# Optimization experiments

Hardware: AMD Instinct MI355X
Metric: run time of the kernel (lower is better)

The kernel has to match this reference:

```python
import jax, jax.numpy as jnp
import numpy as np

D_MODEL = 384
D_INNER = 768
D_STATE = 16
DT_RANK = 24
D_CONV = 4
N_BLOCKS = 6
EPS = 1e-5


def setup_inputs() -> dict:
    key = jax.random.key(0)
    ks = jax.random.split(key, 16)
    s = 0.05
    x = jax.random.normal(ks[0], (1, 8, 16, 16, D_MODEL), jnp.float32)
    inp = {
        'x': x,
        'norm_w': jnp.ones((N_BLOCKS, D_MODEL), jnp.float32),
        'in_proj_w': s * jax.random.normal(ks[1], (N_BLOCKS, 2 * D_INNER, D_MODEL), jnp.float32),
        'conv_w': s * jax.random.normal(ks[2], (N_BLOCKS, D_INNER, D_CONV), jnp.float32),
        'conv_b': jnp.zeros((N_BLOCKS, D_INNER), jnp.float32),
        'x_proj_w': s * jax.random.normal(ks[3], (N_BLOCKS, DT_RANK + 2 * D_STATE, D_INNER), jnp.float32),
        'dt_proj_w': s * jax.random.normal(ks[4], (N_BLOCKS, D_INNER, DT_RANK), jnp.float32),
        'dt_proj_b': jnp.full((N_BLOCKS, D_INNER), -2.0, jnp.float32),  # softplus(-2) ~ small init dt
        'A_log': jnp.broadcast_to(jnp.log(jnp.arange(1, D_STATE + 1, dtype=jnp.float32)), (N_BLOCKS, D_INNER, D_STATE)).copy(),
        'D_param': jnp.ones((N_BLOCKS, D_INNER), jnp.float32),
        'out_proj_w': s * jax.random.normal(ks[5], (N_BLOCKS, D_MODEL, D_INNER), jnp.float32),
    }
    return inp


def _rmsnorm(x, w):
    var = jnp.mean(x * x, axis=-1, keepdims=True)
    return x * jax.lax.rsqrt(var + EPS) * w


def _causal_conv1d(x, w, b):
    # x: (N, L, C), w: (C, k) depthwise, causal left-pad
    xt = jnp.transpose(x, (0, 2, 1))  # (N, C, L)
    out = jax.lax.conv_general_dilated(
        xt, w[:, None, :], window_strides=(1,), padding=[(w.shape[-1] - 1, 0)],
        dimension_numbers=('NCH', 'OIH', 'NCH'), feature_group_count=w.shape[0])
    return jnp.transpose(out, (0, 2, 1)) + b


def _selective_scan(u, delta, A, Bm, Cm, Dp):
    # u, delta: (N, L, d_in); A: (d_in, d_state); Bm, Cm: (N, L, d_state)
    dA = jnp.exp(delta[..., None] * A)                      # (N, L, d_in, d_state)
    dBu = delta[..., None] * Bm[:, :, None, :] * u[..., None]

    def step(h, inp):
        dA_t, dBu_t, C_t = inp
        h = dA_t * h + dBu_t                                # (N, d_in, d_state)
        y = jnp.einsum('nds,ns->nd', h, C_t)
        return h, y

    h0 = jnp.zeros((u.shape[0], u.shape[2], A.shape[1]), u.dtype)
    _, ys = jax.lax.scan(step, h0, (jnp.transpose(dA, (1, 0, 2, 3)),
                                    jnp.transpose(dBu, (1, 0, 2, 3)),
                                    jnp.transpose(Cm, (1, 0, 2))))
    y = jnp.transpose(ys, (1, 0, 2))                        # (N, L, d_in)
    return y + u * Dp


def _mamba_layer(x, p):
    # pre-norm residual Mamba mixer; x: (N, L, D_MODEL)
    h = _rmsnorm(x, p['norm_w'])
    xz = jnp.einsum('nld,ed->nle', h, p['in_proj_w'])       # (N, L, 2*d_inner)
    xp, z = jnp.split(xz, 2, axis=-1)
    xp = jax.nn.silu(_causal_conv1d(xp, p['conv_w'], p['conv_b']))
    x_dbl = jnp.einsum('nld,ed->nle', xp, p['x_proj_w'])
    dt, Bm, Cm = jnp.split(x_dbl, [DT_RANK, DT_RANK + D_STATE], axis=-1)
    dt = jax.nn.softplus(jnp.einsum('nlr,dr->nld', dt, p['dt_proj_w']) + p['dt_proj_b'])
    A = -jnp.exp(p['A_log'])
    y = _selective_scan(xp, dt, A, Bm, Cm, p['D_param'])
    y = y * jax.nn.silu(z)
    return x + jnp.einsum('nle,de->nld', y, p['out_proj_w'])


def _block(x, params, i):
    p = {k: v[i] for k, v in params.items()}
    return _mamba_layer(x, p)


def reference(x, norm_w, in_proj_w, conv_w, conv_b, x_proj_w, dt_proj_w, dt_proj_b, A_log, D_param, out_proj_w):
    params = dict(norm_w=norm_w, in_proj_w=in_proj_w, conv_w=conv_w, conv_b=conv_b,
                  x_proj_w=x_proj_w, dt_proj_w=dt_proj_w, dt_proj_b=dt_proj_b,
                  A_log=A_log, D_param=D_param, out_proj_w=out_proj_w)
    N, L, H, W, D = x.shape
    # HWL ordering
    h = jnp.transpose(x, (0, 2, 3, 1, 4)).reshape(N, H * W * L, D)
    h = _block(h, params, 0)                                 # hwl
    h = _block(h[:, ::-1], params, 1)[:, ::-1]               # r_hwl
    # LWH ordering
    h = h.reshape(N, H, W, L, D)
    h = jnp.transpose(h, (0, 3, 2, 1, 4)).reshape(N, L * W * H, D)
    h = _block(h, params, 2)                                 # lwh
    h = _block(h[:, ::-1], params, 3)[:, ::-1]               # r_lwh
    # LHW ordering
    h = h.reshape(N, L, W, H, D)
    h = jnp.transpose(h, (0, 1, 3, 2, 4)).reshape(N, L * H * W, D)
    h = _block(h, params, 4)                                 # lhw
    h = _block(h[:, ::-1], params, 5)[:, ::-1]               # r_lhw
    return h.reshape(N, L, H, W, D)
```

## Files before the change

kernel.cpp:

```cpp
#include <hip/hip_runtime.h>
#include <math.h>

#define D_MODEL 384
#define D_INNER 768
#define D_STATE 16
#define DT_RANK 24
#define NTOK    2048
#define XDIM    56
#define CHUNK   32
#define NCHUNK  (NTOK / CHUNK)

typedef __attribute__((ext_vector_type(8))) short bf16x8;
typedef __attribute__((ext_vector_type(4))) float f32x4;

__device__ __forceinline__ int tok_of(int order, int p) {
    int q = (order & 1) ? (NTOK - 1 - p) : p;
    int grp = order >> 1;
    int l, h, w;
    if (grp == 0)      { h = q >> 7;  w = (q >> 3) & 15; l = q & 7;  }
    else if (grp == 1) { l = q >> 8;  w = (q >> 4) & 15; h = q & 15; }
    else               { return q; }
    return l * 256 + h * 16 + w;
}

__device__ __forceinline__ float sigmoidf_(float x) { return 1.f / (1.f + expf(-x)); }
__device__ __forceinline__ float softplusf_(float x) { return (x > 20.f) ? x : log1pf(expf(x)); }

__device__ __forceinline__ void bf16split_(float a, unsigned short& hb, unsigned short& lb) {
    unsigned int ab = __float_as_uint(a);
    hb = (unsigned short)(ab >> 16);
    float hf = __uint_as_float(ab & 0xFFFF0000u);
    lb = (unsigned short)(__float_as_uint(a - hf) >> 16);
}

__global__ __launch_bounds__(128) void rmsnorm_gather_k(
    const float* __restrict__ R, const float* __restrict__ nw,
    float* __restrict__ Xn, int order)
{
    const int p   = blockIdx.x;
    const int tok = tok_of(order, p);
    const float* src = R + tok * D_MODEL;
    const int tid = threadIdx.x;
    float v0 = src[tid], v1 = src[tid + 128], v2 = src[tid + 256];
    float ss = v0 * v0 + v1 * v1 + v2 * v2;
#pragma unroll
    for (int off = 32; off > 0; off >>= 1) ss += __shfl_xor(ss, off);
    __shared__ float tot[2];
    if ((tid & 63) == 0) tot[tid >> 6] = ss;
    __syncthreads();
    const float rs = rsqrtf((tot[0] + tot[1]) * (1.f / D_MODEL) + 1e-5f);
    float* dst = Xn + p * D_MODEL;
    dst[tid]       = v0 * rs * nw[tid];
    dst[tid + 128] = v1 * rs * nw[tid + 128];
    dst[tid + 256] = v2 * rs * nw[tid + 256];
}

__global__ __launch_bounds__(256, 3) void inproj_mfma_k(
    const float* __restrict__ Xn, const float* __restrict__ W,
    float* __restrict__ XP, float* __restrict__ GT)
{
    __shared__ __align__(16) short Ah[4 * 64 * 8];
    __shared__ __align__(16) short Al[4 * 64 * 8];
    __shared__ __align__(16) short Bh[4 * 64 * 8];
    __shared__ __align__(16) short Bl[4 * 64 * 8];

    const int tid = threadIdx.x;
    const int m0 = blockIdx.y * 64;
    const int n0 = blockIdx.x * 64;
    const int w  = tid >> 6;
    const int l  = tid & 63;
    const int lr = l & 15;
    const int kg = l >> 4;
    const int srow = tid >> 2;
    const int skq  = tid & 3;

    f32x4 acc[4];
#pragma unroll
    for (int r = 0; r < 4; ++r) acc[r] = (f32x4){0.f, 0.f, 0.f, 0.f};

    for (int k0 = 0; k0 < D_MODEL; k0 += 32) {
        {
            const float* ap = Xn + (m0 + srow) * D_MODEL + k0 + skq * 8;
            const float4 a0 = *(const float4*)ap;
            const float4 a1 = *(const float4*)(ap + 4);
            const float av[8] = {a0.x, a0.y, a0.z, a0.w, a1.x, a1.y, a1.z, a1.w};
            union { bf16x8 v; unsigned short u[8]; } hu, lu;
#pragma unroll
            for (int j = 0; j < 8; ++j) bf16split_(av[j], hu.u[j], lu.u[j]);
            *(bf16x8*)&Ah[(skq * 64 + srow) * 8] = hu.v;
            *(bf16x8*)&Al[(skq * 64 + srow) * 8] = lu.v;

            const float* wp = W + (n0 + srow) * D_MODEL + k0 + skq * 8;
            const float4 w0 = *(const float4*)wp;
            const float4 w1 = *(const float4*)(wp + 4);
            const float wv[8] = {w0.x, w0.y, w0.z, w0.w, w1.x, w1.y, w1.z, w1.w};
            union { bf16x8 v; unsigned short u[8]; } hw, lw;
#pragma unroll
            for (int j = 0; j < 8; ++j) bf16split_(wv[j], hw.u[j], lw.u[j]);
            *(bf16x8*)&Bh[(skq * 64 + srow) * 8] = hw.v;
            *(bf16x8*)&Bl[(skq * 64 + srow) * 8] = lw.v;
        }
        __syncthreads();

        const bf16x8 bh = *(const bf16x8*)&Bh[(kg * 64 + w * 16 + lr) * 8];
        const bf16x8 bl = *(const bf16x8*)&Bl[(kg * 64 + w * 16 + lr) * 8];
#pragma unroll
        for (int r = 0; r < 4; ++r) {
            const bf16x8 ah = *(const bf16x8*)&Ah[(kg * 64 + r * 16 + lr) * 8];
            const bf16x8 al = *(const bf16x8*)&Al[(kg * 64 + r * 16 + lr) * 8];
            acc[r] = __builtin_amdgcn_mfma_f32_16x16x32_bf16(ah, bh, acc[r], 0, 0, 0);
            acc[r] = __builtin_amdgcn_mfma_f32_16x16x32_bf16(ah, bl, acc[r], 0, 0, 0);
            acc[r] = __builtin_amdgcn_mfma_f32_16x16x32_bf16(al, bh, acc[r], 0, 0, 0);
        }
        __syncthreads();
    }

    const int n = n0 + w * 16 + lr;
    if (n0 < D_INNER) {
#pragma unroll
        for (int r = 0; r < 4; ++r)
#pragma unroll
            for (int i = 0; i < 4; ++i) {
                const int t = m0 + r * 16 + kg * 4 + i;
                XP[t * D_INNER + n] = acc[r][i];
            }
    } else {
        const int n2 = n - D_INNER;
#pragma unroll
        for (int r = 0; r < 4; ++r)
#pragma unroll
            for (int i = 0; i < 4; ++i) {
                const int t = m0 + r * 16 + kg * 4 + i;
                const float c = acc[r][i];
                GT[n2 * NTOK + t] = c * sigmoidf_(c);
            }
    }
}

template<int MODE, bool TRANSA>
__global__ __launch_bounds__(256, 2) void gemm_k(
    const float* __restrict__ A, int lda,
    const float* __restrict__ W,
    float* __restrict__ C,
    int M, int N, int K,
    const float* __restrict__ bias,
    float* __restrict__ C2,
    int kspan)
{
    __shared__ float As[16][68];
    __shared__ float Ws[16][68];
    const int tid = threadIdx.x;
    const int m0 = blockIdx.y * 64;
    const int n0 = blockIdx.x * 64;
    const int tx = tid & 15, ty = tid >> 4;
    const int lrow = tid >> 2;
    const int lk   = (tid & 3) << 2;
    const int kb   = blockIdx.z * kspan;
    const int ke   = (kb + kspan < K) ? (kb + kspan) : K;
    float acc[4][4] = {{0.f}};

    for (int k0 = kb; k0 < ke; k0 += 16) {
        if (TRANSA) {
            const int kk = k0 + (tid & 15);
            const int mq = tid >> 4;
            float4 v = make_float4(0.f, 0.f, 0.f, 0.f);
            if (kk < K) v = *(const float4*)&A[kk * lda + m0 + mq * 4];
            *(float4*)&As[tid & 15][mq * 4] = v;
        } else {
            const int m = m0 + lrow;
            const float* src = A + m * lda + (k0 + lk);
            float4 v = make_float4(0.f, 0.f, 0.f, 0.f);
            if (k0 + lk + 3 < K) v = *(const float4*)src;
            else {
                if (k0 + lk + 0 < K) v.x = src[0];
                if (k0 + lk + 1 < K) v.y = src[1];
                if (k0 + lk + 2 < K) v.z = src[2];
            }
            As[lk + 0][lrow] = v.x; As[lk + 1][lrow] = v.y;
            As[lk + 2][lrow] = v.z; As[lk + 3][lrow] = v.w;
        }
        {
            const int n = n0 + lrow;
            float4 u = make_float4(0.f, 0.f, 0.f, 0.f);
            if (n < N) {
                const float* srcw = W + n * K + (k0 + lk);
                if (k0 + lk + 3 < K) u = *(const float4*)srcw;
                else {
                    if (k0 + lk + 0 < K) u.x = srcw[0];
                    if (k0 + lk + 1 < K) u.y = srcw[1];
                    if (k0 + lk + 2 < K) u.z = srcw[2];
                }
            }
            Ws[lk + 0][lrow] = u.x; Ws[lk + 1][lrow] = u.y;
            Ws[lk + 2][lrow] = u.z; Ws[lk + 3][lrow] = u.w;
        }
        __syncthreads();
#pragma unroll
        for (int k = 0; k < 16; ++k) {
            float4 a4 = *(const float4*)&As[k][ty * 4];
            float4 w4 = *(const float4*)&Ws[k][tx * 4];
            float ar[4] = {a4.x, a4.y, a4.z, a4.w};
            float wr[4] = {w4.x, w4.y, w4.z, w4.w};
#pragma unroll
            for (int i = 0; i < 4; ++i)
#pragma unroll
                for (int j = 0; j < 4; ++j)
                    acc[i][j] = fmaf(ar[i], wr[j], acc[i][j]);
        }
        __syncthreads();
    }

    const int row0 = m0 + ty * 4;
    const int col0 = n0 + tx * 4;
    if (MODE == 0) {
        float* Cz = C + (size_t)blockIdx.z * M * N;
#pragma unroll
        for (int i = 0; i < 4; ++i) {
            float4 v = make_float4(acc[i][0], acc[i][1], acc[i][2], acc[i][3]);
            *(float4*)&Cz[(row0 + i) * N + col0] = v;
        }
    } else if (MODE == 3) {
        float* Cz = C + (size_t)blockIdx.z * N * NTOK;
#pragma unroll
        for (int j = 0; j < 4; ++j) {
            const int col = col0 + j;
            if (col < N) {
                float4 v = make_float4(acc[0][j], acc[1][j], acc[2][j], acc[3][j]);
                *(float4*)&Cz[col * NTOK + row0] = v;
            }
        }
    } else if (MODE == 4) {
#pragma unroll
        for (int j = 0; j < 4; ++j) {
            const int col = col0 + j;
            if (col < N) {
                const float bv = bias[col];
                float4 v = make_float4(softplusf_(acc[0][j] + bv), softplusf_(acc[1][j] + bv),
                                       softplusf_(acc[2][j] + bv), softplusf_(acc[3][j] + bv));
                *(float4*)&C[col * NTOK + row0] = v;
            }
        }
    }
}

__global__ __launch_bounds__(256) void reduce_px_k(
    const float* __restrict__ PX, float* __restrict__ XDT)
{
    const int i4 = blockIdx.x * 256 + threadIdx.x;
    float4 s = ((const float4*)PX)[i4];
#pragma unroll
    for (int z = 1; z < 8; ++z) {
        float4 v = ((const float4*)PX)[z * (XDIM * NTOK / 4) + i4];
        s.x += v.x; s.y += v.y; s.z += v.z; s.w += v.w;
    }
    ((float4*)XDT)[i4] = s;
}

__global__ __launch_bounds__(384) void reduce_scatter_k(
    const float* __restrict__ PO, float* __restrict__ R, int order)
{
    const int m = blockIdx.x;
    const int col = threadIdx.x;
    float s = PO[m * D_MODEL + col];
#pragma unroll
    for (int z = 1; z < 4; ++z)
        s += PO[z * (NTOK * D_MODEL) + m * D_MODEL + col];
    const int tok = tok_of(order, m);
    R[tok * D_MODEL + col] += s;
}

__global__ __launch_bounds__(256) void conv_silu_t_k(
    const float* __restrict__ XP, const float* __restrict__ cw,
    const float* __restrict__ cb, float* __restrict__ XCT)
{
    __shared__ float xs[67][33];
    const int c0 = blockIdx.x * 32;
    const int t0 = blockIdx.y * 64;
    const int tid = threadIdx.x;
    const int col = tid & 31, rr = tid >> 5;
#pragma unroll
    for (int r = rr; r < 67; r += 8) {
        const int t = t0 - 3 + r;
        xs[r][col] = (t >= 0) ? XP[t * D_INNER + c0 + col] : 0.f;
    }
    __syncthreads();
    const int tl = tid & 63;
#pragma unroll
    for (int cl = tid >> 6; cl < 32; cl += 4) {
        const int c = c0 + cl;
        const float4 w4 = *(const float4*)(cw + c * 4);
        float acc = cb[c];
        acc = fmaf(w4.x, xs[tl + 0][cl], acc);
        acc = fmaf(w4.y, xs[tl + 1][cl], acc);
        acc = fmaf(w4.z, xs[tl + 2][cl], acc);
        acc = fmaf(w4.w, xs[tl + 3][cl], acc);
        XCT[c * NTOK + t0 + tl] = acc * sigmoidf_(acc);
    }
}

__global__ __launch_bounds__(256) void scan_phase1_k(
    const float* __restrict__ XCT, const float* __restrict__ DTT,
    const float* __restrict__ XDT, const float* __restrict__ A_log,
    float* __restrict__ Aprod, float* __restrict__ Hpart)
{
    const int tid = threadIdx.x;
    const int s = tid & 15;
    const int d = blockIdx.x * 16 + (tid >> 4);
    const int chunk = blockIdx.y;
    const float Aneg = -expf(A_log[d * D_STATE + s]);
    const float* dtp = DTT + d * NTOK + chunk * CHUNK;
    const float* up  = XCT + d * NTOK + chunk * CHUNK;
    const float* Bp  = XDT + (DT_RANK + s) * NTOK + chunk * CHUNK;
    float h = 0.f, ap = 1.f;
#pragma unroll
    for (int tt = 0; tt < CHUNK; tt += 4) {
        const float4 dt4 = *(const float4*)(dtp + tt);
        const float4 u4  = *(const float4*)(up + tt);
        const float4 B4  = *(const float4*)(Bp + tt);
        float a;
        a = expf(dt4.x * Aneg); h = fmaf(a, h, dt4.x * B4.x * u4.x); ap *= a;
        a = expf(dt4.y * Aneg); h = fmaf(a, h, dt4.y * B4.y * u4.y); ap *= a;
        a = expf(dt4.z * Aneg); h = fmaf(a, h, dt4.z * B4.z * u4.z); ap *= a;
        a = expf(dt4.w * Aneg); h = fmaf(a, h, dt4.w * B4.w * u4.w); ap *= a;
    }
    const int idx = (chunk * D_INNER + d) * D_STATE + s;
    Aprod[idx] = ap;
    Hpart[idx] = h;
}

__global__ __launch_bounds__(256) void scan_phase2_k(
    const float* __restrict__ Aprod, const float* __restrict__ Hpart,
    float* __restrict__ Hinit)
{
    const int tid = blockIdx.x * 256 + threadIdx.x;
    float h = 0.f;
#pragma unroll 8
    for (int c = 0; c < NCHUNK; ++c) {
        const int idx = c * (D_INNER * D_STATE) + tid;
        Hinit[idx] = h;
        h = fmaf(Aprod[idx], h, Hpart[idx]);
    }
}

__global__ __launch_bounds__(256) void scan_phase3_k(
    const float* __restrict__ XCT, const float* __restrict__ DTT,
    const float* __restrict__ XDT, const float* __restrict__ GT,
    const float* __restrict__ A_log, const float* __restrict__ Dp,
    const float* __restrict__ Hinit, float* __restrict__ YGT)
{
    const int tid = threadIdx.x;
    const int s = tid & 15;
    const int d = blockIdx.x * 16 + (tid >> 4);
    const int chunk = blockIdx.y;
    const float Aneg = -expf(A_log[d * D_STATE + s]);
    const float Dv = Dp[d];
    const float* dtp = DTT + d * NTOK + chunk * CHUNK;
    const float* up  = XCT + d * NTOK + chunk * CHUNK;
    const float* Bp  = XDT + (DT_RANK + s) * NTOK + chunk * CHUNK;
    const float* Cp  = XDT + (DT_RANK + D_STATE + s) * NTOK + chunk * CHUNK;
    const float* Gp  = GT  + d * NTOK + chunk * CHUNK;
    float* Yp        = YGT + d * NTOK + chunk * CHUNK;
    float h = Hinit[(chunk * D_INNER + d) * D_STATE + s];
#pragma unroll
    for (int tt = 0; tt < CHUNK; tt += 4) {
        const float4 dt4 = *(const float4*)(dtp + tt);
        const float4 u4  = *(const float4*)(up + tt);
        const float4 B4  = *(const float4*)(Bp + tt);
        const float4 C4  = *(const float4*)(Cp + tt);
        float a, p0, p1, p2, p3;
        a = expf(dt4.x * Aneg); h = fmaf(a, h, dt4.x * B4.x * u4.x); p0 = h * C4.x;
        a = expf(dt4.y * Aneg); h = fmaf(a, h, dt4.y * B4.y * u4.y); p1 = h * C4.y;
        a = expf(dt4.z * Aneg); h = fmaf(a, h, dt4.z * B4.z * u4.z); p2 = h * C4.z;
        a = expf(dt4.w * Aneg); h = fmaf(a, h, dt4.w * B4.w * u4.w); p3 = h * C4.w;
#pragma unroll
        for (int m = 1; m <= 8; m <<= 1) {
            p0 += __shfl_xor(p0, m); p1 += __shfl_xor(p1, m);
            p2 += __shfl_xor(p2, m); p3 += __shfl_xor(p3, m);
        }
        if (s == 0) {
            const float4 g4 = *(const float4*)(Gp + tt);
            float4 y;
            y.x = (p0 + u4.x * Dv) * g4.x;
            y.y = (p1 + u4.y * Dv) * g4.y;
            y.z = (p2 + u4.z * Dv) * g4.z;
            y.w = (p3 + u4.w * Dv) * g4.w;
            *(float4*)(Yp + tt) = y;
        }
    }
}

extern "C" void kernel_launch(void* const* d_in, const int* in_sizes, int n_in,
                              void* d_out, int out_size, void* d_ws, size_t ws_size,
                              hipStream_t stream)
{
    const float* x        = (const float*)d_in[0];
    const float* norm_w   = (const float*)d_in[1];
    const float* in_proj  = (const float*)d_in[2];
    const float* conv_w   = (const float*)d_in[3];
    const float* conv_b   = (const float*)d_in[4];
    const float* x_proj   = (const float*)d_in[5];
    const float* dt_proj  = (const float*)d_in[6];
    const float* dt_b     = (const float*)d_in[7];
    const float* A_log    = (const float*)d_in[8];
    const float* D_param  = (const float*)d_in[9];
    const float* out_proj = (const float*)d_in[10];

    float* ws = (float*)d_ws;
    float* R     = ws;
    float* XP    = R   + 786432;
    float* Xn    = XP  + 1572864;
    float* GT    = Xn  + 786432;
    float* XCT   = GT  + 1572864;
    float* XDT   = XCT + 1572864;
    float* DTT   = XDT + 114688;
    float* YGT   = DTT + 1572864;
    float* Aprod = Xn;
    float* Hpart = YGT;
    float* Hinit = XP;
    float* PX    = XP;
    float* PO    = GT;

    hipMemcpyAsync(R, x, (size_t)786432 * sizeof(float), hipMemcpyDeviceToDevice, stream);

    for (int b = 0; b < 6; ++b) {
        rmsnorm_gather_k<<<NTOK, 128, 0, stream>>>(R, norm_w + b * D_MODEL, Xn, b);

        inproj_mfma_k<<<dim3(24, 32), 256, 0, stream>>>(
            Xn, in_proj + (size_t)b * 2 * D_INNER * D_MODEL, XP, GT);

        conv_silu_t_k<<<dim3(24, 32), 256, 0, stream>>>(
            XP, conv_w + b * D_INNER * 4, conv_b + b * D_INNER, XCT);

        gemm_k<3, true><<<dim3(1, 32, 8), 256, 0, stream>>>(
            XCT, NTOK, x_proj + (size_t)b * XDIM * D_INNER, PX,
            NTOK, XDIM, D_INNER, nullptr, nullptr, 96);

        reduce_px_k<<<112, 256, 0, stream>>>(PX, XDT);

        gemm_k<4, true><<<dim3(12, 32, 1), 256, 0, stream>>>(
            XDT, NTOK, dt_proj + (size_t)b * D_INNER * DT_RANK, DTT,
            NTOK, D_INNER, DT_RANK, dt_b + b * D_INNER, nullptr, DT_RANK);

        scan_phase1_k<<<dim3(48, NCHUNK), 256, 0, stream>>>(
            XCT, DTT, XDT, A_log + (size_t)b * D_INNER * D_STATE, Aprod, Hpart);

        scan_phase2_k<<<48, 256, 0, stream>>>(Aprod, Hpart, Hinit);

        scan_phase3_k<<<dim3(48, NCHUNK), 256, 0, stream>>>(
            XCT, DTT, XDT, GT, A_log + (size_t)b * D_INNER * D_STATE,
            D_param + b * D_INNER, Hinit, YGT);

        gemm_k<0, true><<<dim3(6, 32, 4), 256, 0, stream>>>(
            YGT, NTOK, out_proj + (size_t)b * D_MODEL * D_INNER, PO,
            NTOK, D_MODEL, D_INNER, nullptr, nullptr, 192);

        reduce_scatter_k<<<NTOK, 384, 0, stream>>>(PO, R, b);
    }

    hipMemcpyAsync(d_out, R, (size_t)786432 * sizeof(float), hipMemcpyDeviceToDevice, stream);
}
```

Measured before the change: 937.1 us.

## Pre-split weights to bf16 hi/lo and move out_proj to MFMA

Adds a presplit kernel that converts the in_proj and out_proj weights into bf16 high/low pairs once per call. RMSNorm now writes the split activations directly, so the in_proj MFMA kernel only copies bf16 data into shared memory. The out_proj GEMM moves from the fp32 FMA kernel to a new split-bf16 MFMA kernel with split-K of 2 instead of 4. To support that, the scan writes Y token-major, which turns its float4 stores into strided scalar stores, and the extra weight buffers need more workspace.

```diff
diff --git a/kernel.cpp b/kernel.cpp
--- a/kernel.cpp
+++ b/kernel.cpp
@@ -33,9 +33,25 @@
     lb = (unsigned short)(__float_as_uint(a - hf) >> 16);
 }
 
+__global__ __launch_bounds__(256) void presplit_k(
+    const float* __restrict__ A, unsigned short* __restrict__ H,
+    unsigned short* __restrict__ L, int n4)
+{
+    const int i = blockIdx.x * 256 + threadIdx.x;
+    if (i >= n4) return;
+    const float4 v = ((const float4*)A)[i];
+    ushort4 h, l;
+    bf16split_(v.x, h.x, l.x);
+    bf16split_(v.y, h.y, l.y);
+    bf16split_(v.z, h.z, l.z);
+    bf16split_(v.w, h.w, l.w);
+    ((ushort4*)H)[i] = h;
+    ((ushort4*)L)[i] = l;
+}
+
 __global__ __launch_bounds__(128) void rmsnorm_gather_k(
     const float* __restrict__ R, const float* __restrict__ nw,
-    float* __restrict__ Xn, int order)
+    unsigned short* __restrict__ Xnh, unsigned short* __restrict__ Xnl, int order)
 {
     const int p   = blockIdx.x;
     const int tok = tok_of(order, p);
@@ -49,14 +65,18 @@
     if ((tid & 63) == 0) tot[tid >> 6] = ss;
     __syncthreads();
     const float rs = rsqrtf((tot[0] + tot[1]) * (1.f / D_MODEL) + 1e-5f);
-    float* dst = Xn + p * D_MODEL;
-    dst[tid]       = v0 * rs * nw[tid];
-    dst[tid + 128] = v1 * rs * nw[tid + 128];
-    dst[tid + 256] = v2 * rs * nw[tid + 256];
+    unsigned short h, l;
+    bf16split_(v0 * rs * nw[tid], h, l);
+    Xnh[p * D_MODEL + tid] = h;       Xnl[p * D_MODEL + tid] = l;
+    bf16split_(v1 * rs * nw[tid + 128], h, l);
+    Xnh[p * D_MODEL + tid + 128] = h; Xnl[p * D_MODEL + tid + 128] = l;
+    bf16split_(v2 * rs * nw[tid + 256], h, l);
+    Xnh[p * D_MODEL + tid + 256] = h; Xnl[p * D_MODEL + tid + 256] = l;
 }
 
 __global__ __launch_bounds__(256, 3) void inproj_mfma_k(
-    const float* __restrict__ Xn, const float* __restrict__ W,
+    const unsigned short* __restrict__ Ahg, const unsigned short* __restrict__ Alg,
+    const unsigned short* __restrict__ WH, const unsigned short* __restrict__ WL,
     float* __restrict__ XP, float* __restrict__ GT)
 {
     __shared__ __align__(16) short Ah[4 * 64 * 8];
@@ -79,27 +99,13 @@
     for (int r = 0; r < 4; ++r) acc[r] = (f32x4){0.f, 0.f, 0.f, 0.f};
 
     for (int k0 = 0; k0 < D_MODEL; k0 += 32) {
-        {
-            const float* ap = Xn + (m0 + srow) * D_MODEL + k0 + skq * 8;
-            const float4 a0 = *(const float4*)ap;
-            const float4 a1 = *(const float4*)(ap + 4);
-            const float av[8] = {a0.x, a0.y, a0.z, a0.w, a1.x, a1.y, a1.z, a1.w};
-            union { bf16x8 v; unsigned short u[8]; } hu, lu;
-#pragma unroll
-            for (int j = 0; j < 8; ++j) bf16split_(av[j], hu.u[j], lu.u[j]);
-            *(bf16x8*)&Ah[(skq * 64 + srow) * 8] = hu.v;
-            *(bf16x8*)&Al[(skq * 64 + srow) * 8] = lu.v;
-
-            const float* wp = W + (n0 + srow) * D_MODEL + k0 + skq * 8;
-            const float4 w0 = *(const float4*)wp;
-            const float4 w1 = *(const float4*)(wp + 4);
-            const float wv[8] = {w0.x, w0.y, w0.z, w0.w, w1.x, w1.y, w1.z, w1.w};
-            union { bf16x8 v; unsigned short u[8]; } hw, lw;
-#pragma unroll
-            for (int j = 0; j < 8; ++j) bf16split_(wv[j], hw.u[j], lw.u[j]);
-            *(bf16x8*)&Bh[(skq * 64 + srow) * 8] = hw.v;
-            *(bf16x8*)&Bl[(skq * 64 + srow) * 8] = lw.v;
-        }
+        const int aoff = (m0 + srow) * D_MODEL + k0 + skq * 8;
+        const int woff = (n0 + srow) * D_MODEL + k0 + skq * 8;
+        const int soff = (skq * 64 + srow) * 8;
+        *(bf16x8*)&Ah[soff] = *(const bf16x8*)&Ahg[aoff];
+        *(bf16x8*)&Al[soff] = *(const bf16x8*)&Alg[aoff];
+        *(bf16x8*)&Bh[soff] = *(const bf16x8*)&WH[woff];
+        *(bf16x8*)&Bl[soff] = *(const bf16x8*)&WL[woff];
         __syncthreads();
 
         const bf16x8 bh = *(const bf16x8*)&Bh[(kg * 64 + w * 16 + lr) * 8];
@@ -135,6 +141,70 @@
                 GT[n2 * NTOK + t] = c * sigmoidf_(c);
             }
     }
+}
+
+__global__ __launch_bounds__(256, 3) void outproj_mfma_k(
+    const float* __restrict__ YG, const unsigned short* __restrict__ WH,
+    const unsigned short* __restrict__ WL, float* __restrict__ PO)
+{
+    __shared__ __align__(16) short Ah[4 * 64 * 8];
+    __shared__ __align__(16) short Al[4 * 64 * 8];
+    __shared__ __align__(16) short Bh[4 * 64 * 8];
+    __shared__ __align__(16) short Bl[4 * 64 * 8];
+
+    const int tid = threadIdx.x;
+    const int m0 = blockIdx.y * 64;
+    const int n0 = blockIdx.x * 64;
+    const int kb = blockIdx.z * 384;
+    const int w  = tid >> 6;
+    const int l  = tid & 63;
+    const int lr = l & 15;
+    const int kg = l >> 4;
+    const int srow = tid >> 2;
+    const int skq  = tid & 3;
+
+    f32x4 acc[4];
+#pragma unroll
+    for (int r = 0; r < 4; ++r) acc[r] = (f32x4){0.f, 0.f, 0.f, 0.f};
+
+    for (int k0 = 0; k0 < 384; k0 += 32) {
+        const float* ap = YG + (m0 + srow) * D_INNER + kb + k0 + skq * 8;
+        const float4 a0 = *(const float4*)ap;
+        const float4 a1 = *(const float4*)(ap + 4);
+        const float av[8] = {a0.x, a0.y, a0.z, a0.w, a1.x, a1.y, a1.z, a1.w};
+        union { bf16x8 v; unsigned short u[8]; } hu, lu;
+#pragma unroll
+        for (int j = 0; j < 8; ++j) bf16split_(av[j], hu.u[j], lu.u[j]);
+        const int soff = (skq * 64 + srow) * 8;
+        *(bf16x8*)&Ah[soff] = hu.v;
+        *(bf16x8*)&Al[soff] = lu.v;
+        const int woff = (n0 + srow) * D_INNER + kb + k0 + skq * 8;
+        *(bf16x8*)&Bh[soff] = *(const bf16x8*)&WH[woff];
+        *(bf16x8*)&Bl[soff] = *(const bf16x8*)&WL[woff];
+        __syncthreads();
+
+        const bf16x8 bh = *(const bf16x8*)&Bh[(kg * 64 + w * 16 + lr) * 8];
+        const bf16x8 bl = *(const bf16x8*)&Bl[(kg * 64 + w * 16 + lr) * 8];
+#pragma unroll
+        for (int r = 0; r < 4; ++r) {
+            const bf16x8 ah = *(const bf16x8*)&Ah[(kg * 64 + r * 16 + lr) * 8];
+            const bf16x8 al = *(const bf16x8*)&Al[(kg * 64 + r * 16 + lr) * 8];
+            acc[r] = __builtin_amdgcn_mfma_f32_16x16x32_bf16(ah, bh, acc[r], 0, 0, 0);
+            acc[r] = __builtin_amdgcn_mfma_f32_16x16x32_bf16(ah, bl, acc[r], 0, 0, 0);
+            acc[r] = __builtin_amdgcn_mfma_f32_16x16x32_bf16(al, bh, acc[r], 0, 0, 0);
+        }
+        __syncthreads();
+    }
+
+    float* Cz = PO + (size_t)blockIdx.z * NTOK * D_MODEL;
+    const int n = n0 + w * 16 + lr;
+#pragma unroll
+    for (int r = 0; r < 4; ++r)
+#pragma unroll
+        for (int i = 0; i < 4; ++i) {
+            const int t = m0 + r * 16 + kg * 4 + i;
+            Cz[t * D_MODEL + n] = acc[r][i];
+        }
 }
 
 template<int MODE, bool TRANSA>
@@ -212,14 +282,7 @@
 
     const int row0 = m0 + ty * 4;
     const int col0 = n0 + tx * 4;
-    if (MODE == 0) {
-        float* Cz = C + (size_t)blockIdx.z * M * N;
-#pragma unroll
-        for (int i = 0; i < 4; ++i) {
-            float4 v = make_float4(acc[i][0], acc[i][1], acc[i][2], acc[i][3]);
-            *(float4*)&Cz[(row0 + i) * N + col0] = v;
-        }
-    } else if (MODE == 3) {
+    if (MODE == 3) {
         float* Cz = C + (size_t)blockIdx.z * N * NTOK;
 #pragma unroll
         for (int j = 0; j < 4; ++j) {
@@ -261,10 +324,7 @@
 {
     const int m = blockIdx.x;
     const int col = threadIdx.x;
-    float s = PO[m * D_MODEL + col];
-#pragma unroll
-    for (int z = 1; z < 4; ++z)
-        s += PO[z * (NTOK * D_MODEL) + m * D_MODEL + col];
+    float s = PO[m * D_MODEL + col] + PO[NTOK * D_MODEL + m * D_MODEL + col];
     const int tok = tok_of(order, m);
     R[tok * D_MODEL + col] += s;
 }
@@ -346,7 +406,7 @@
     const float* __restrict__ XCT, const float* __restrict__ DTT,
     const float* __restrict__ XDT, const float* __restrict__ GT,
     const float* __restrict__ A_log, const float* __restrict__ Dp,
-    const float* __restrict__ Hinit, float* __restrict__ YGT)
+    const float* __restrict__ Hinit, float* __restrict__ YG)
 {
     const int tid = threadIdx.x;
     const int s = tid & 15;
@@ -359,7 +419,6 @@
     const float* Bp  = XDT + (DT_RANK + s) * NTOK + chunk * CHUNK;
     const float* Cp  = XDT + (DT_RANK + D_STATE + s) * NTOK + chunk * CHUNK;
     const float* Gp  = GT  + d * NTOK + chunk * CHUNK;
-    float* Yp        = YGT + d * NTOK + chunk * CHUNK;
     float h = Hinit[(chunk * D_INNER + d) * D_STATE + s];
 #pragma unroll
     for (int tt = 0; tt < CHUNK; tt += 4) {
@@ -379,12 +438,11 @@
         }
         if (s == 0) {
             const float4 g4 = *(const float4*)(Gp + tt);
-            float4 y;
-            y.x = (p0 + u4.x * Dv) * g4.x;
-            y.y = (p1 + u4.y * Dv) * g4.y;
-            y.z = (p2 + u4.z * Dv) * g4.z;
-            y.w = (p3 + u4.w * Dv) * g4.w;
-            *(float4*)(Yp + tt) = y;
+            const int tbase = chunk * CHUNK + tt;
+            YG[(tbase + 0) * D_INNER + d] = (p0 + u4.x * Dv) * g4.x;
+            YG[(tbase + 1) * D_INNER + d] = (p1 + u4.y * Dv) * g4.y;
+            YG[(tbase + 2) * D_INNER + d] = (p2 + u4.z * Dv) * g4.z;
+            YG[(tbase + 3) * D_INNER + d] = (p3 + u4.w * Dv) * g4.w;
         }
     }
 }
@@ -408,25 +466,37 @@
     float* ws = (float*)d_ws;
     float* R     = ws;
     float* XP    = R   + 786432;
-    float* Xn    = XP  + 1572864;
-    float* GT    = Xn  + 786432;
+    float* XnHL  = XP  + 1572864;
+    float* GT    = XnHL + 786432;
     float* XCT   = GT  + 1572864;
     float* XDT   = XCT + 1572864;
     float* DTT   = XDT + 114688;
-    float* YGT   = DTT + 1572864;
-    float* Aprod = Xn;
-    float* Hpart = YGT;
+    float* YG    = DTT + 1572864;
+    float* WS1   = YG  + 1572864;
+    unsigned short* Xnh  = (unsigned short*)XnHL;
+    unsigned short* Xnl  = Xnh + 786432;
+    unsigned short* WinH = (unsigned short*)WS1;
+    unsigned short* WinL = WinH + 6 * 1536 * 384;
+    unsigned short* WoutH = WinL + 6 * 1536 * 384;
+    unsigned short* WoutL = WoutH + 6 * 384 * 768;
+    float* Aprod = XnHL;
+    float* Hpart = YG;
     float* Hinit = XP;
     float* PX    = XP;
     float* PO    = GT;
 
     hipMemcpyAsync(R, x, (size_t)786432 * sizeof(float), hipMemcpyDeviceToDevice, stream);
 
+    presplit_k<<<(6 * 1536 * 384 / 4 + 255) / 256, 256, 0, stream>>>(
+        in_proj, WinH, WinL, 6 * 1536 * 384 / 4);
+    presplit_k<<<(6 * 384 * 768 / 4 + 255) / 256, 256, 0, stream>>>(
+        out_proj, WoutH, WoutL, 6 * 384 * 768 / 4);
+
     for (int b = 0; b < 6; ++b) {
-        rmsnorm_gather_k<<<NTOK, 128, 0, stream>>>(R, norm_w + b * D_MODEL, Xn, b);
+        rmsnorm_gather_k<<<NTOK, 128, 0, stream>>>(R, norm_w + b * D_MODEL, Xnh, Xnl, b);
 
         inproj_mfma_k<<<dim3(24, 32), 256, 0, stream>>>(
-            Xn, in_proj + (size_t)b * 2 * D_INNER * D_MODEL, XP, GT);
+            Xnh, Xnl, WinH + (size_t)b * 1536 * 384, WinL + (size_t)b * 1536 * 384, XP, GT);
 
         conv_silu_t_k<<<dim3(24, 32), 256, 0, stream>>>(
             XP, conv_w + b * D_INNER * 4, conv_b + b * D_INNER, XCT);
@@ -448,11 +518,10 @@
 
         scan_phase3_k<<<dim3(48, NCHUNK), 256, 0, stream>>>(
             XCT, DTT, XDT, GT, A_log + (size_t)b * D_INNER * D_STATE,
-            D_param + b * D_INNER, Hinit, YGT);
-
-        gemm_k<0, true><<<dim3(6, 32, 4), 256, 0, stream>>>(
-            YGT, NTOK, out_proj + (size_t)b * D_MODEL * D_INNER, PO,
-            NTOK, D_MODEL, D_INNER, nullptr, nullptr, 192);
+            D_param + b * D_INNER, Hinit, YG);
+
+        outproj_mfma_k<<<dim3(6, 32, 2), 256, 0, stream>>>(
+            YG, WoutH + (size_t)b * 384 * 768, WoutL + (size_t)b * 384 * 768, PO);
 
         reduce_scatter_k<<<NTOK, 384, 0, stream>>>(PO, R, b);
     }
```

Result: faster. 900.8 us (-3.9%).
